# Kernel optimization log

Measured on AMD Instinct MI355X. Metric: run time of the kernel, lower is better.

The kernel has to match this reference:

```python
import jax, jax.numpy as jnp
import numpy as np

# LIF constants matching SpikingLinearLayer defaults
DT = 1.0
TAU_M = 20.0
TAU_S = 5.0
THRESH = 1.0
SURR_BETA = 10.0  # surrogate sigmoid sharpness


def _spike(v):
    """Hard threshold forward, sigmoid surrogate gradient (straight-through)."""
    s_hard = (v >= 0.0).astype(v.dtype)
    s_surr = jax.nn.sigmoid(SURR_BETA * v)
    return s_surr + jax.lax.stop_gradient(s_hard - s_surr)


def setup_inputs() -> dict:
    key = jax.random.key(0)
    k1, k2 = jax.random.split(key)
    T, B, IN, OUT = 20, 1024, 2048, 2048
    x = (jax.random.uniform(k1, (T, B, IN)) < 0.1).astype(jnp.float32)
    # nn.init.normal_(weight, mu=0.1, std=0.1)
    weight = 0.1 + 0.1 * jax.random.normal(k2, (OUT, IN), dtype=jnp.float32)
    return {"x": x, "weight": weight}


def reference(x, weight):
    # x: [T, B, in_dim] spike trains; weight: [out_dim, in_dim]
    alpha_m = 1.0 - DT / TAU_M  # membrane decay
    alpha_s = 1.0 - DT / TAU_S  # synaptic decay
    # batch all timestep GEMMs into one contraction: [T, B, out]
    cur = jnp.einsum("tbi,oi->tbo", x, weight)
    B, O = cur.shape[1], cur.shape[2]
    V0 = jnp.zeros((B, O), cur.dtype)
    I0 = jnp.zeros((B, O), cur.dtype)

    def step(carry, c_t):
        V, I = carry
        I = alpha_s * I + c_t                   # tau_s dI/dt = -I + W s_in
        V = alpha_m * V + (DT / TAU_M) * I      # tau_m dV/dt = -V + I
        s = _spike(V - THRESH)                  # fire at threshold
        V = V * (1.0 - s)                       # reset to zero on spike
        return (V, I), s

    _, spikes = jax.lax.scan(step, (V0, I0), cur)
    return spikes  # [T, B, out_dim]
```

## Files before the change

kernel.cpp:

```cpp
#include <hip/hip_runtime.h>
#include <stdint.h>


constexpr int T_STEPS = 20;
constexpr int BATCH   = 1024;
constexpr int NIN     = 2048;
constexpr int NOUT    = 2048;

constexpr int    Q         = 4;
constexpr double SCALE     = 1073741824.0;
constexpr double INV_SCALE = 1.0 / SCALE;

constexpr size_t XIP_BYTES   = (size_t)T_STEPS * 16 * 1024 * 16;
constexpr size_t PLANE_BYTES = (size_t)NOUT * NIN;
constexpr size_t WS_NEEDED   = XIP_BYTES + (size_t)Q * PLANE_BYTES;

typedef int v4i __attribute__((ext_vector_type(4)));

__device__ __forceinline__ void dma16(const int8_t* g, const int8_t* l) {
    __builtin_amdgcn_global_load_lds(
        (const __attribute__((address_space(1))) void*)(uintptr_t)g,
        (__attribute__((address_space(3))) void*)(uint32_t)(uintptr_t)l,
        16, 0, 0);
}

__device__ __forceinline__ v4i expand16(uint32_t b) {
    v4i r;
    r[0] = (int)((((b      ) & 0xFu) * 0x00204081u) & 0x01010101u);
    r[1] = (int)((((b >>  4) & 0xFu) * 0x00204081u) & 0x01010101u);
    r[2] = (int)((((b >>  8) & 0xFu) * 0x00204081u) & 0x01010101u);
    r[3] = (int)((((b >> 12) & 0xFu) * 0x00204081u) & 0x01010101u);
    return r;
}

__global__ void prep_x(const float* __restrict__ x, int8_t* __restrict__ xp) {
    const int tid  = threadIdx.x;
    const int ln   = tid & 63;
    const int row  = blockIdx.x * 4 + (tid >> 6);
    const int t    = row >> 10;
    const int b    = row & 1023;
    const float* xr = x + (size_t)row * NIN;
#pragma unroll
    for (int c = 0; c < 32; ++c) {
        const unsigned long long m = __ballot(xr[c * 64 + ln] != 0.0f);
        if (ln == 0)
            *reinterpret_cast<unsigned long long*>(
                xp + (((size_t)t * 16 + (c >> 1)) * 1024 + b) * 16
                   + (c & 1) * 8) = m;
    }
}

__global__ void prep_limbs(const float* __restrict__ w, int8_t* __restrict__ limbs) {
    const int idx = blockIdx.x * blockDim.x + threadIdx.x;
    const float4 wv = reinterpret_cast<const float4*>(w)[idx];
    const float wf[4] = {wv.x, wv.y, wv.z, wv.w};
    int8_t d[Q][4];
#pragma unroll
    for (int e = 0; e < 4; ++e) {
        long long M = llrint((double)wf[e] * SCALE);
#pragma unroll
        for (int j = 0; j < Q - 1; ++j) {
            const int dj = (int)((M + 128) & 255) - 128;
            d[j][e] = (int8_t)dj;
            M = (M - dj) >> 8;
        }
        d[Q - 1][e] = (int8_t)M;
    }
#pragma unroll
    for (int j = 0; j < Q; ++j)
        reinterpret_cast<char4*>(limbs + (size_t)j * PLANE_BYTES)[idx] =
            make_char4(d[j][0], d[j][1], d[j][2], d[j][3]);
}

constexpr int KC2    = 128;
constexpr int NKC2   = NIN / KC2;
constexpr int TT     = 4;
constexpr int NTQ    = T_STEPS / TT;
constexpr int NITER  = NTQ * NKC2;
constexpr int BM     = 256;
constexpr int BO     = 16;
constexpr int B_OFF  = 16384;
constexpr int BUF_B  = 24576;

__global__ __launch_bounds__(512, 2)
void snn_i8(const int8_t* __restrict__ xp, const int8_t* __restrict__ limbs,
            float* __restrict__ out)
{
    const int bid   = blockIdx.x;
    const int xcd   = bid & 7;
    const int sub   = bid >> 3;
    const int otile = xcd * 16 + (sub & 15);
    const int btile = sub >> 4;
    const int o0 = otile * BO, b0 = btile * BM;

    const int tid = threadIdx.x;
    const int w   = tid >> 6;
    const int ln  = tid & 63;
    const int lm  = ln & 15;
    const int qd  = ln >> 4;

    __shared__ __align__(16) int8_t lds[2][BUF_B];

    const int sa_tt = w >> 1;
    const int sa_g  = (w & 1) * 2;
    const int sb_j  = w >> 1;
    const int sb_h  = w & 1;

    const size_t b_src = (size_t)sb_j * PLANE_BYTES
                       + (size_t)(o0 + lm) * NIN + sb_h * 64 + qd * 16;

    double V[8], I[8];
#pragma unroll
    for (int e = 0; e < 8; ++e) { V[e] = 0.0; I[e] = 0.0; }

    const double alpha_m = 1.0 - 1.0 / 20.0;
    const double alpha_s = 1.0 - 1.0 / 5.0;
    const double dtm     = 1.0 / 20.0;

    auto stage = [&](int s) {
        const int tq  = s >> 4;
        const int kc2 = s & 15;
        int8_t* lb = &lds[s & 1][0];
        const size_t abase =
            (((size_t)(tq * 4 + sa_tt) * 16 + kc2) * 1024 + b0) * 16;
        dma16(xp + abase + (size_t)(sa_g * 64 + ln) * 16,
              lb + (sa_tt * 4 + sa_g) * 1024);
        dma16(xp + abase + (size_t)((sa_g + 1) * 64 + ln) * 16,
              lb + (sa_tt * 4 + sa_g + 1) * 1024);
        dma16(limbs + b_src + (size_t)kc2 * KC2,
              lb + B_OFF + (sb_j * 2 + sb_h) * 1024);
    };

    stage(0);
    __syncthreads();

    int s = 0;
    for (int tq = 0; tq < NTQ; ++tq) {
        v4i acc[2][4][4];
#pragma unroll
        for (int rg2 = 0; rg2 < 2; ++rg2)
#pragma unroll
            for (int tt = 0; tt < TT; ++tt)
#pragma unroll
                for (int j = 0; j < Q; ++j)
                    acc[rg2][tt][j] = (v4i){0, 0, 0, 0};

        for (int kci = 0; kci < NKC2; ++kci, ++s) {
            if (s + 1 < NITER) stage(s + 1);

            const int8_t* cb = &lds[s & 1][0];
#pragma unroll
            for (int s2 = 0; s2 < 2; ++s2) {
                v4i B[4];
#pragma unroll
                for (int j = 0; j < Q; ++j)
                    B[j] = *reinterpret_cast<const v4i*>(
                        cb + B_OFF + ((j * 2 + s2) * 64 + ln) * 16);
#pragma unroll
                for (int rg2 = 0; rg2 < 2; ++rg2) {
                    const int r = (2 * w + rg2) * 16 + lm;
#pragma unroll
                    for (int tt = 0; tt < TT; ++tt) {
                        const uint32_t bits =
                            *reinterpret_cast<const uint16_t*>(
                                cb + tt * 4096 + r * 16 + s2 * 8 + qd * 2);
                        const v4i A = expand16(bits);
#pragma unroll
                        for (int j = 0; j < Q; ++j)
                            acc[rg2][tt][j] =
                                __builtin_amdgcn_mfma_i32_16x16x64_i8(
                                    A, B[j], acc[rg2][tt][j], 0, 0, 0);
                    }
                }
            }
            __syncthreads();
        }

        const int ocol = o0 + lm;
#pragma unroll
        for (int rg2 = 0; rg2 < 2; ++rg2) {
#pragma unroll
            for (int r = 0; r < 4; ++r) {
                const int e = rg2 * 4 + r;
                const int brow = b0 + (2 * w + rg2) * 16 + 4 * qd + r;
#pragma unroll
                for (int tt = 0; tt < TT; ++tt) {
                    const int d0 = acc[rg2][tt][0][r];
                    const int d1 = acc[rg2][tt][1][r];
                    const int d2 = acc[rg2][tt][2][r];
                    const int d3 = acc[rg2][tt][3][r];
                    double sm = (double)d3;
                    sm = sm * 256.0 + (double)d2;
                    sm = sm * 256.0 + (double)d1;
                    sm = sm * 256.0 + (double)d0;
                    const double cur = sm * INV_SCALE;

                    I[e] = alpha_s * I[e] + cur;
                    V[e] = alpha_m * V[e] + dtm * I[e];
                    const double sp = (V[e] >= 1.0) ? 1.0 : 0.0;
                    V[e] *= (1.0 - sp);

                    __builtin_nontemporal_store(
                        (float)sp,
                        out + (size_t)(tq * 4 + tt) * BATCH * NOUT
                            + (size_t)brow * NOUT + ocol);
                }
            }
        }
    }
}

constexpr int TBF = 64, TOF = 64, KCF = 64, LDPF = KCF + 4;

__global__ __launch_bounds__(256, 2)
void snn_fused(const float* __restrict__ x,
               const float* __restrict__ w,
               float* __restrict__ out)
{
    const int o0  = blockIdx.x * TOF;
    const int b0  = blockIdx.y * TBF;
    const int tid = threadIdx.x;
    const int tx  = tid & 15;
    const int ty  = tid >> 4;

    __shared__ float xs[TBF][LDPF];
    __shared__ float ws[TOF][LDPF];

    const int lr = tid >> 2;
    const int lc = (tid & 3) << 4;

    double V[4][4], I[4][4];
#pragma unroll
    for (int i = 0; i < 4; ++i)
#pragma unroll
        for (int j = 0; j < 4; ++j) { V[i][j] = 0.0; I[i][j] = 0.0; }

    const double alpha_m = 1.0 - 1.0 / 20.0;
    const double alpha_s = 1.0 - 1.0 / 5.0;
    const double dtm     = 1.0 / 20.0;

    for (int t = 0; t < T_STEPS; ++t) {
        const float* xt = x + (size_t)t * BATCH * NIN;
        double c[4][4];
#pragma unroll
        for (int i = 0; i < 4; ++i)
#pragma unroll
            for (int j = 0; j < 4; ++j) c[i][j] = 0.0;

        for (int kc = 0; kc < NIN; kc += KCF) {
            __syncthreads();
            {
                const float4* xg = reinterpret_cast<const float4*>(
                    xt + (size_t)(b0 + lr) * NIN + kc + lc);
                const float4* wg = reinterpret_cast<const float4*>(
                    w + (size_t)(o0 + lr) * NIN + kc + lc);
#pragma unroll
                for (int q = 0; q < 4; ++q) {
                    float4 xv = xg[q];
                    float4 wv4 = wg[q];
                    const int cbi = lc + q * 4;
                    xs[lr][cbi + 0] = xv.x;  xs[lr][cbi + 1] = xv.y;
                    xs[lr][cbi + 2] = xv.z;  xs[lr][cbi + 3] = xv.w;
                    ws[lr][cbi + 0] = wv4.x; ws[lr][cbi + 1] = wv4.y;
                    ws[lr][cbi + 2] = wv4.z; ws[lr][cbi + 3] = wv4.w;
                }
            }
            __syncthreads();

#pragma unroll 8
            for (int k = 0; k < KCF; ++k) {
                float xa[4], wa[4];
#pragma unroll
                for (int i = 0; i < 4; ++i) xa[i] = xs[ty * 4 + i][k];
#pragma unroll
                for (int j = 0; j < 4; ++j) wa[j] = ws[tx * 4 + j][k];
#pragma unroll
                for (int i = 0; i < 4; ++i)
#pragma unroll
                    for (int j = 0; j < 4; ++j)
                        c[i][j] += (double)xa[i] * (double)wa[j];
            }
        }

#pragma unroll
        for (int i = 0; i < 4; ++i) {
            float sv[4];
#pragma unroll
            for (int j = 0; j < 4; ++j) {
                I[i][j] = alpha_s * I[i][j] + c[i][j];
                V[i][j] = alpha_m * V[i][j] + dtm * I[i][j];
                const double sp = (V[i][j] >= 1.0) ? 1.0 : 0.0;
                V[i][j] *= (1.0 - sp);
                sv[j] = (float)sp;
            }
            const size_t oidx = (size_t)t * BATCH * NOUT
                              + (size_t)(b0 + ty * 4 + i) * NOUT
                              + (size_t)(o0 + tx * 4);
            *reinterpret_cast<float4*>(out + oidx) =
                make_float4(sv[0], sv[1], sv[2], sv[3]);
        }
    }
}

extern "C" void kernel_launch(void* const* d_in, const int* in_sizes, int n_in,
                              void* d_out, int out_size, void* d_ws, size_t ws_size,
                              hipStream_t stream) {
    const float* x = (const float*)d_in[0];
    const float* w = (const float*)d_in[1];
    float* out     = (float*)d_out;
    (void)in_sizes; (void)n_in; (void)out_size;

    if (ws_size >= WS_NEEDED) {
        int8_t* xp    = (int8_t*)d_ws;
        int8_t* limbs = xp + XIP_BYTES;
        prep_x<<<5120, 256, 0, stream>>>(x, xp);
        prep_limbs<<<(int)(PLANE_BYTES / 4 / 256), 256, 0, stream>>>(w, limbs);
        snn_i8<<<512, 512, 0, stream>>>(xp, limbs, out);
    } else {
        dim3 grid(NOUT / TOF, BATCH / TBF);
        snn_fused<<<grid, dim3(256), 0, stream>>>(x, w, out);
    }
}
```

Measured before the change: 556.2 us.

## Shrink i8 GEMM tile to 128 rows and 2 timesteps with 256-thread blocks

Retiles the int8 limb-GEMM spiking kernel: each block now covers 128 batch rows and processes 2 timesteps per pass instead of 256 rows and 4 timesteps, using 4 waves of 256 threads. The LDS staging layout and DMA assignment are reworked so each wave loads one weight limb plane, and the grid doubles to 1024 blocks with a 3-blocks-per-CU launch bound. The aim is more resident blocks and smaller accumulator and LDS footprints for better occupancy and latency hiding. In exchange each block reloads the weight tile more often relative to the work it does, and the K loop repeats 10 times instead of 5.

```diff
diff --git a/kernel.cpp b/kernel.cpp
--- a/kernel.cpp
+++ b/kernel.cpp
@@ -72,17 +72,17 @@
             make_char4(d[j][0], d[j][1], d[j][2], d[j][3]);
 }
 
-constexpr int KC2    = 128;
-constexpr int NKC2   = NIN / KC2;
-constexpr int TT     = 4;
-constexpr int NTQ    = T_STEPS / TT;
-constexpr int NITER  = NTQ * NKC2;
-constexpr int BM     = 256;
+constexpr int KC     = 128;
+constexpr int NKC    = NIN / KC;
+constexpr int TT     = 2;
+constexpr int NTP    = T_STEPS / TT;
+constexpr int NITER  = NTP * NKC;
+constexpr int BM     = 128;
 constexpr int BO     = 16;
-constexpr int B_OFF  = 16384;
-constexpr int BUF_B  = 24576;
-
-__global__ __launch_bounds__(512, 2)
+constexpr int B_OFF  = 4096;
+constexpr int BUF_B  = 12288;
+
+__global__ __launch_bounds__(256, 3)
 void snn_i8(const int8_t* __restrict__ xp, const int8_t* __restrict__ limbs,
             float* __restrict__ out)
 {
@@ -102,12 +102,9 @@
     __shared__ __align__(16) int8_t lds[2][BUF_B];
 
     const int sa_tt = w >> 1;
-    const int sa_g  = (w & 1) * 2;
-    const int sb_j  = w >> 1;
-    const int sb_h  = w & 1;
-
-    const size_t b_src = (size_t)sb_j * PLANE_BYTES
-                       + (size_t)(o0 + lm) * NIN + sb_h * 64 + qd * 16;
+    const int sa_h  = w & 1;
+    const size_t b_src = (size_t)w * PLANE_BYTES
+                       + (size_t)(o0 + lm) * NIN + qd * 16;
 
     double V[8], I[8];
 #pragma unroll
@@ -118,25 +115,24 @@
     const double dtm     = 1.0 / 20.0;
 
     auto stage = [&](int s) {
-        const int tq  = s >> 4;
-        const int kc2 = s & 15;
+        const int tp = s >> 4;
+        const int kc = s & 15;
         int8_t* lb = &lds[s & 1][0];
-        const size_t abase =
-            (((size_t)(tq * 4 + sa_tt) * 16 + kc2) * 1024 + b0) * 16;
-        dma16(xp + abase + (size_t)(sa_g * 64 + ln) * 16,
-              lb + (sa_tt * 4 + sa_g) * 1024);
-        dma16(xp + abase + (size_t)((sa_g + 1) * 64 + ln) * 16,
-              lb + (sa_tt * 4 + sa_g + 1) * 1024);
-        dma16(limbs + b_src + (size_t)kc2 * KC2,
-              lb + B_OFF + (sb_j * 2 + sb_h) * 1024);
+        dma16(xp + (((size_t)(2 * tp + sa_tt) * 16 + kc) * 1024
+                    + b0 + sa_h * 64 + ln) * 16,
+              lb + sa_tt * 2048 + sa_h * 1024);
+#pragma unroll
+        for (int s2 = 0; s2 < 2; ++s2)
+            dma16(limbs + b_src + (size_t)kc * KC + s2 * 64,
+                  lb + B_OFF + (w * 2 + s2) * 1024);
     };
 
     stage(0);
     __syncthreads();
 
     int s = 0;
-    for (int tq = 0; tq < NTQ; ++tq) {
-        v4i acc[2][4][4];
+    for (int tp = 0; tp < NTP; ++tp) {
+        v4i acc[2][2][4];
 #pragma unroll
         for (int rg2 = 0; rg2 < 2; ++rg2)
 #pragma unroll
@@ -145,7 +141,7 @@
                 for (int j = 0; j < Q; ++j)
                     acc[rg2][tt][j] = (v4i){0, 0, 0, 0};
 
-        for (int kci = 0; kci < NKC2; ++kci, ++s) {
+        for (int kci = 0; kci < NKC; ++kci, ++s) {
             if (s + 1 < NITER) stage(s + 1);
 
             const int8_t* cb = &lds[s & 1][0];
@@ -155,15 +151,15 @@
 #pragma unroll
                 for (int j = 0; j < Q; ++j)
                     B[j] = *reinterpret_cast<const v4i*>(
-                        cb + B_OFF + ((j * 2 + s2) * 64 + ln) * 16);
+                        cb + B_OFF + (j * 2 + s2) * 1024 + ln * 16);
 #pragma unroll
                 for (int rg2 = 0; rg2 < 2; ++rg2) {
-                    const int r = (2 * w + rg2) * 16 + lm;
+                    const int row = 32 * w + rg2 * 16 + lm;
 #pragma unroll
                     for (int tt = 0; tt < TT; ++tt) {
                         const uint32_t bits =
                             *reinterpret_cast<const uint16_t*>(
-                                cb + tt * 4096 + r * 16 + s2 * 8 + qd * 2);
+                                cb + tt * 2048 + row * 16 + s2 * 8 + qd * 2);
                         const v4i A = expand16(bits);
 #pragma unroll
                         for (int j = 0; j < Q; ++j)
@@ -202,7 +198,7 @@
 
                     __builtin_nontemporal_store(
                         (float)sp,
-                        out + (size_t)(tq * 4 + tt) * BATCH * NOUT
+                        out + (size_t)(2 * tp + tt) * BATCH * NOUT
                             + (size_t)brow * NOUT + ocol);
                 }
             }
@@ -315,7 +311,7 @@
         int8_t* limbs = xp + XIP_BYTES;
         prep_x<<<5120, 256, 0, stream>>>(x, xp);
         prep_limbs<<<(int)(PLANE_BYTES / 4 / 256), 256, 0, stream>>>(w, limbs);
-        snn_i8<<<512, 512, 0, stream>>>(xp, limbs, out);
+        snn_i8<<<1024, 256, 0, stream>>>(xp, limbs, out);
     } else {
         dim3 grid(NOUT / TOF, BATCH / TBF);
         snn_fused<<<grid, dim3(256), 0, stream>>>(x, w, out);
```

Measured after the change: 566.6 us. Within noise of the previous version (+1.9%).
